# Optimization experiments

Hardware: AMD Instinct MI355X
Metric: run time of the kernel (lower is better)

The kernel has to match this reference:

```python
import jax, jax.numpy as jnp
import numpy as np

# ---- social-force / MPDM constants (param object in the original) ----
N = 4096           # number of agents (row 0 = robot)
DT = 0.4           # integration timestep [s]
PED_SPEED = 1.0    # desired pedestrian speed [m/s]
K_ATTR = 2.0       # attractive-force gain k
ALPHA = 10.0       # repulsive-force amplitude
PED_RADIUS = 0.3   # pedestrian radius [m]
PED_MASS = 60.0    # pedestrian mass [kg]
BETTA = 0.71       # repulsion range constant
A_COST = 5.0       # deviation (blame) weight a
B_COST = 2.0       # proximity-blame weight b
E_COST = 1.0       # blame length scale e
EPS = 1e-8


def calc_forces(state, goal):
    pos, vel = state[:, :2], state[:, 2:4]
    # attractive force toward goal: k * (v_desired - v_current)
    to_goal = goal - pos
    dist_g = jnp.sqrt(jnp.sum(to_goal * to_goal, axis=1, keepdims=True) + EPS)
    af = K_ATTR * (PED_SPEED * to_goal / dist_g - vel)
    # pairwise repulsive social force, [N,N,2] interaction tensor
    delta = pos[:, None, :] - pos[None, :, :]                 # [N,N,2]
    dist = jnp.sqrt(jnp.sum(delta * delta, axis=-1) + EPS)    # [N,N]
    mag = ALPHA * jnp.exp((2.0 * PED_RADIUS - dist) / BETTA)  # [N,N]
    mag = mag * (1.0 - jnp.eye(pos.shape[0], dtype=pos.dtype))  # no self-force
    rf = jnp.einsum('ij,ijc->ic', mag / dist, delta) / PED_MASS
    return rf, af


def pose_propagation(F, state):
    pos, vel = state[:, :2], state[:, 2:4]
    new_pos = pos + vel * DT + 0.5 * F * (DT * DT)
    new_vel = vel + F * DT
    spd = jnp.sqrt(jnp.sum(new_vel * new_vel, axis=1, keepdims=True) + EPS)
    new_vel = new_vel * jnp.minimum(1.0, PED_SPEED / spd)  # clamp to max speed
    return jnp.concatenate([new_pos, new_vel], axis=1)


def calc_cost_function(goal, robot_init_pose, out_state, observed_state):
    robot_pose = out_state[0, :2]
    peds = out_state[1:, :2]
    obs = observed_state[1:, :2]
    # progress of robot toward its goal
    pg = (jnp.sqrt(jnp.sum((robot_init_pose - goal[0]) ** 2) + EPS)
          - jnp.sqrt(jnp.sum((robot_pose - goal[0]) ** 2) + EPS))
    # blame: pedestrian deviation from observed trajectory
    deviation = jnp.sum(jnp.sqrt(jnp.sum((peds - obs) ** 2, axis=1) + EPS))
    # blame: robot proximity to pedestrians
    d = jnp.sqrt(jnp.sum((peds - robot_pose) ** 2, axis=1) + EPS)
    blame = jnp.sum(jnp.exp(-d / E_COST))
    return A_COST * deviation + B_COST * blame - pg


def setup_inputs() -> dict:
    key = jax.random.key(0)
    k1, k2, k3, k4 = jax.random.split(key, 4)
    pos = jax.random.normal(k1, (N, 2), dtype=jnp.float32) * 20.0
    vel = jax.random.normal(k2, (N, 2), dtype=jnp.float32)
    state = jnp.concatenate([pos, vel], axis=1)
    goal = jax.random.normal(k3, (N, 2), dtype=jnp.float32) * 20.0
    obs_pos = pos + 0.1 * jax.random.normal(k4, (N, 2), dtype=jnp.float32)
    observed_state = jnp.concatenate([obs_pos, vel], axis=1)
    return {
        'state': state,
        'cost': jnp.zeros((1,), dtype=jnp.float32),
        'stacked_trajectories_for_visualizer': state,
        'goal': goal,
        'observed_state': observed_state,
    }


def reference(state, cost, stacked_trajectories_for_visualizer, goal, observed_state):
    rf, af = calc_forces(state, goal)
    F = rf + af
    output = pose_propagation(F, state)
    temp = calc_cost_function(goal, state[0, :2], output, observed_state)
    new_cost = cost + temp
    stacked = jnp.concatenate([stacked_trajectories_for_visualizer, state], axis=0)
    return (output, new_cost, stacked)
```

## Files before the change

### kernel.cpp

```cpp
#include <hip/hip_runtime.h>

#define NPED 4096
#define SPLIT 32
#define JC (NPED / SPLIT)
#define BI 256
#define EPSF 1e-8f
#define DTF 0.4f
#define INV_MASS (1.0f/60.0f)
#define C1f (-2.0319648463225964f)
#define C0f (4.54110700268092f)
#define NLOG2E (-1.4426950408889634f)

typedef float f2 __attribute__((ext_vector_type(2)));

__device__ __forceinline__ float rsqf(float x) { return __builtin_amdgcn_rsqf(x); }
__device__ __forceinline__ float ex2(float x)  { return __builtin_amdgcn_exp2f(x); }

__global__ __launch_bounds__(BI) void forces_kernel(const float4* __restrict__ state,
                                                    const float* __restrict__ cost_in,
                                                    f2* __restrict__ part,
                                                    float* __restrict__ out) {
    __shared__ f2 spos[JC];
    const int t  = threadIdx.x;
    const int ib = blockIdx.x & 15;
    const int s  = blockIdx.x >> 4;
    if (t < JC) {
        float4 r = state[s * JC + t];
        spos[t] = (f2){r.x, r.y};
    }
    if (blockIdx.x == 0 && t == 0) out[NPED * 4] = cost_in[0];
    const int i = ib * BI + t;
    float4 mest = state[i];
    __syncthreads();
    const f2 me = {mest.x, mest.y};
    f2 acc = {0.f, 0.f};
    #pragma unroll 8
    for (int j = 0; j < JC; ++j) {
        f2 d = me - spos[j];
        float d2 = fmaf(d.x, d.x, fmaf(d.y, d.y, EPSF));
        float inv = rsqf(d2);
        float dist = d2 * inv;
        float w = ex2(fmaf(dist, C1f, C0f)) * inv;
        acc = d * w + acc;
    }
    part[s * NPED + i] = acc;
}

__device__ __forceinline__ float4 integrate_one(float4 st, float2 g,
                                                float fx, float fy) {
    fx *= INV_MASS; fy *= INV_MASS;
    float tx = g.x - st.x, ty = g.y - st.y;
    float invg = rsqf(fmaf(tx, tx, fmaf(ty, ty, EPSF)));
    float Fx = fx + 2.f * fmaf(tx, invg, -st.z);
    float Fy = fy + 2.f * fmaf(ty, invg, -st.w);
    float npx = fmaf(0.08f, Fx, fmaf(DTF, st.z, st.x));
    float npy = fmaf(0.08f, Fy, fmaf(DTF, st.w, st.y));
    float nvx = fmaf(DTF, Fx, st.z);
    float nvy = fmaf(DTF, Fy, st.w);
    float invs = rsqf(fmaf(nvx, nvx, fmaf(nvy, nvy, EPSF)));
    float sc = fminf(1.f, invs);
    return make_float4(npx, npy, nvx * sc, nvy * sc);
}

__global__ __launch_bounds__(BI) void finish_kernel(const float4* __restrict__ state,
                                                    const float2* __restrict__ goal,
                                                    const float4* __restrict__ stk,
                                                    const float* __restrict__ obs,
                                                    const f2* __restrict__ part,
                                                    float* __restrict__ out) {
    const int t  = threadIdx.x;
    const int b  = blockIdx.x;
    const int ii = b * BI + t;

    f2 f = {0.f, 0.f};
    #pragma unroll
    for (int sp = 0; sp < SPLIT; ++sp) f += part[sp * NPED + ii];
    float4 st = state[ii];
    float4 nw = integrate_one(st, goal[ii], f.x, f.y);
    ((float4*)out)[ii] = nw;

    float4 sv = stk[ii];
    float* o1 = out + (NPED * 4 + 1) + ii * 4;
    o1[0] = sv.x; o1[1] = sv.y; o1[2] = sv.z; o1[3] = sv.w;
    float* o2 = o1 + NPED * 4;
    o2[0] = st.x; o2[1] = st.y; o2[2] = st.z; o2[3] = st.w;

    __shared__ float2 rpose;
    if (t < 64) {
        f2 rf = {0.f, 0.f};
        if (t < SPLIT) rf = part[t * NPED];
        #pragma unroll
        for (int off = 16; off > 0; off >>= 1) {
            rf.x += __shfl_down(rf.x, off);
            rf.y += __shfl_down(rf.y, off);
        }
        if (t == 0) {
            float4 r0 = integrate_one(state[0], goal[0], rf.x, rf.y);
            rpose = make_float2(r0.x, r0.y);
        }
    }
    __syncthreads();
    const float rx = rpose.x, ry = rpose.y;

    float c = 0.f;
    if (ii >= 1) {
        float ox = obs[ii * 4 + 0], oy = obs[ii * 4 + 1];
        float dxo = nw.x - ox, dyo = nw.y - oy;
        float dev = sqrtf(fmaf(dxo, dxo, fmaf(dyo, dyo, EPSF)));
        float dxr = nw.x - rx, dyr = nw.y - ry;
        float d = sqrtf(fmaf(dxr, dxr, fmaf(dyr, dyr, EPSF)));
        float blame = ex2(NLOG2E * d);
        c = fmaf(5.f, dev, 2.f * blame);
    }
    #pragma unroll
    for (int off = 32; off > 0; off >>= 1) c += __shfl_down(c, off);
    __shared__ float sc4[4];
    if ((t & 63) == 0) sc4[t >> 6] = c;
    __syncthreads();
    if (t == 0) {
        float total = sc4[0] + sc4[1] + sc4[2] + sc4[3];
        if (b == 0) {
            const float* stf = (const float*)state;
            const float* gf  = (const float*)goal;
            float gx = gf[0], gy = gf[1];
            float a1x = stf[0] - gx, a1y = stf[1] - gy;
            float a2x = rx - gx,     a2y = ry - gy;
            float pg = sqrtf(fmaf(a1x, a1x, fmaf(a1y, a1y, EPSF)))
                     - sqrtf(fmaf(a2x, a2x, fmaf(a2y, a2y, EPSF)));
            total -= pg;
        }
        atomicAdd(out + NPED * 4, total);
    }
}

extern "C" void kernel_launch(void* const* d_in, const int* in_sizes, int n_in,
                              void* d_out, int out_size, void* d_ws, size_t ws_size,
                              hipStream_t stream) {
    const float4* state = (const float4*)d_in[0];
    const float*  cost  = (const float*)d_in[1];
    const float4* stk   = (const float4*)d_in[2];
    const float2* goal  = (const float2*)d_in[3];
    const float*  obs   = (const float*)d_in[4];
    float* out = (float*)d_out;
    f2* part = (f2*)d_ws;

    forces_kernel<<<dim3(16 * SPLIT), BI, 0, stream>>>(state, cost, part, out);
    finish_kernel<<<dim3(16), BI, 0, stream>>>(state, goal, stk, obs, part, out);
}
```

Before: 73.30 us.

## Split pair sum across warp lanes, fuse integration, single-block cost reduction

```diff
diff --git a/kernel.cpp b/kernel.cpp
--- a/kernel.cpp
+++ b/kernel.cpp
@@ -1,9 +1,8 @@
 #include <hip/hip_runtime.h>
 
 #define NPED 4096
-#define SPLIT 32
-#define JC (NPED / SPLIT)
 #define BI 256
+#define IPB 8
 #define EPSF 1e-8f
 #define DTF 0.4f
 #define INV_MASS (1.0f/60.0f)
@@ -15,36 +14,6 @@
 
 __device__ __forceinline__ float rsqf(float x) { return __builtin_amdgcn_rsqf(x); }
 __device__ __forceinline__ float ex2(float x)  { return __builtin_amdgcn_exp2f(x); }
-
-__global__ __launch_bounds__(BI) void forces_kernel(const float4* __restrict__ state,
-                                                    const float* __restrict__ cost_in,
-                                                    f2* __restrict__ part,
-                                                    float* __restrict__ out) {
-    __shared__ f2 spos[JC];
-    const int t  = threadIdx.x;
-    const int ib = blockIdx.x & 15;
-    const int s  = blockIdx.x >> 4;
-    if (t < JC) {
-        float4 r = state[s * JC + t];
-        spos[t] = (f2){r.x, r.y};
-    }
-    if (blockIdx.x == 0 && t == 0) out[NPED * 4] = cost_in[0];
-    const int i = ib * BI + t;
-    float4 mest = state[i];
-    __syncthreads();
-    const f2 me = {mest.x, mest.y};
-    f2 acc = {0.f, 0.f};
-    #pragma unroll 8
-    for (int j = 0; j < JC; ++j) {
-        f2 d = me - spos[j];
-        float d2 = fmaf(d.x, d.x, fmaf(d.y, d.y, EPSF));
-        float inv = rsqf(d2);
-        float dist = d2 * inv;
-        float w = ex2(fmaf(dist, C1f, C0f)) * inv;
-        acc = d * w + acc;
-    }
-    part[s * NPED + i] = acc;
-}
 
 __device__ __forceinline__ float4 integrate_one(float4 st, float2 g,
                                                 float fx, float fy) {
@@ -62,74 +31,87 @@
     return make_float4(npx, npy, nvx * sc, nvy * sc);
 }
 
-__global__ __launch_bounds__(BI) void finish_kernel(const float4* __restrict__ state,
+__global__ __launch_bounds__(BI) void forces_kernel(const float4* __restrict__ state,
                                                     const float2* __restrict__ goal,
                                                     const float4* __restrict__ stk,
-                                                    const float* __restrict__ obs,
-                                                    const f2* __restrict__ part,
                                                     float* __restrict__ out) {
-    const int t  = threadIdx.x;
-    const int b  = blockIdx.x;
-    const int ii = b * BI + t;
+    __shared__ f2 spos[NPED];
+    const int t = threadIdx.x;
+    #pragma unroll
+    for (int k = 0; k < NPED / BI; ++k) {
+        float4 r = state[k * BI + t];
+        spos[k * BI + t] = (f2){r.x, r.y};
+    }
+    const int jl = t & 31;
+    const int i  = blockIdx.x * IPB + (t >> 5);
+    float4 st = state[i];
+    __syncthreads();
 
-    f2 f = {0.f, 0.f};
+    const f2 me = {st.x, st.y};
+    f2 acc = {0.f, 0.f};
+    #pragma unroll 8
+    for (int k = 0; k < NPED / 32; ++k) {
+        f2 d = me - spos[(k << 5) + jl];
+        float d2 = fmaf(d.x, d.x, fmaf(d.y, d.y, EPSF));
+        float inv = rsqf(d2);
+        float dist = d2 * inv;
+        float w = ex2(fmaf(dist, C1f, C0f)) * inv;
+        acc = d * w + acc;
+    }
     #pragma unroll
-    for (int sp = 0; sp < SPLIT; ++sp) f += part[sp * NPED + ii];
-    float4 st = state[ii];
-    float4 nw = integrate_one(st, goal[ii], f.x, f.y);
-    ((float4*)out)[ii] = nw;
+    for (int off = 16; off > 0; off >>= 1) {
+        acc.x += __shfl_xor(acc.x, off);
+        acc.y += __shfl_xor(acc.y, off);
+    }
+    if (jl == 0) {
+        float4 nw = integrate_one(st, goal[i], acc.x, acc.y);
+        ((float4*)out)[i] = nw;
+        float4 sv = stk[i];
+        float* o1 = out + (NPED * 4 + 1) + i * 4;
+        o1[0] = sv.x; o1[1] = sv.y; o1[2] = sv.z; o1[3] = sv.w;
+        float* o2 = o1 + NPED * 4;
+        o2[0] = st.x; o2[1] = st.y; o2[2] = st.z; o2[3] = st.w;
+    }
+}
 
-    float4 sv = stk[ii];
-    float* o1 = out + (NPED * 4 + 1) + ii * 4;
-    o1[0] = sv.x; o1[1] = sv.y; o1[2] = sv.z; o1[3] = sv.w;
-    float* o2 = o1 + NPED * 4;
-    o2[0] = st.x; o2[1] = st.y; o2[2] = st.z; o2[3] = st.w;
-
-    __shared__ float2 rpose;
-    if (t < 64) {
-        f2 rf = {0.f, 0.f};
-        if (t < SPLIT) rf = part[t * NPED];
-        #pragma unroll
-        for (int off = 16; off > 0; off >>= 1) {
-            rf.x += __shfl_down(rf.x, off);
-            rf.y += __shfl_down(rf.y, off);
+__global__ __launch_bounds__(1024) void cost_kernel(const float4* __restrict__ state,
+                                                    const float2* __restrict__ goal,
+                                                    const float4* __restrict__ obs,
+                                                    const float* __restrict__ cost_in,
+                                                    float* __restrict__ out) {
+    const int t = threadIdx.x;
+    const float rx = out[0], ry = out[1];
+    float c = 0.f;
+    #pragma unroll
+    for (int k = 0; k < NPED / 1024; ++k) {
+        const int i = (k << 10) + t;
+        if (i >= 1) {
+            float4 nw = ((const float4*)out)[i];
+            float4 ob = obs[i];
+            float dxo = nw.x - ob.x, dyo = nw.y - ob.y;
+            float dev = sqrtf(fmaf(dxo, dxo, fmaf(dyo, dyo, EPSF)));
+            float dxr = nw.x - rx, dyr = nw.y - ry;
+            float d = sqrtf(fmaf(dxr, dxr, fmaf(dyr, dyr, EPSF)));
+            c = fmaf(5.f, dev, fmaf(2.f, ex2(NLOG2E * d), c));
         }
-        if (t == 0) {
-            float4 r0 = integrate_one(state[0], goal[0], rf.x, rf.y);
-            rpose = make_float2(r0.x, r0.y);
-        }
-    }
-    __syncthreads();
-    const float rx = rpose.x, ry = rpose.y;
-
-    float c = 0.f;
-    if (ii >= 1) {
-        float ox = obs[ii * 4 + 0], oy = obs[ii * 4 + 1];
-        float dxo = nw.x - ox, dyo = nw.y - oy;
-        float dev = sqrtf(fmaf(dxo, dxo, fmaf(dyo, dyo, EPSF)));
-        float dxr = nw.x - rx, dyr = nw.y - ry;
-        float d = sqrtf(fmaf(dxr, dxr, fmaf(dyr, dyr, EPSF)));
-        float blame = ex2(NLOG2E * d);
-        c = fmaf(5.f, dev, 2.f * blame);
     }
     #pragma unroll
     for (int off = 32; off > 0; off >>= 1) c += __shfl_down(c, off);
-    __shared__ float sc4[4];
-    if ((t & 63) == 0) sc4[t >> 6] = c;
+    __shared__ float wsum[16];
+    if ((t & 63) == 0) wsum[t >> 6] = c;
     __syncthreads();
     if (t == 0) {
-        float total = sc4[0] + sc4[1] + sc4[2] + sc4[3];
-        if (b == 0) {
-            const float* stf = (const float*)state;
-            const float* gf  = (const float*)goal;
-            float gx = gf[0], gy = gf[1];
-            float a1x = stf[0] - gx, a1y = stf[1] - gy;
-            float a2x = rx - gx,     a2y = ry - gy;
-            float pg = sqrtf(fmaf(a1x, a1x, fmaf(a1y, a1y, EPSF)))
-                     - sqrtf(fmaf(a2x, a2x, fmaf(a2y, a2y, EPSF)));
-            total -= pg;
-        }
-        atomicAdd(out + NPED * 4, total);
+        float tot = 0.f;
+        #pragma unroll
+        for (int w = 0; w < 16; ++w) tot += wsum[w];
+        const float* stf = (const float*)state;
+        const float* gf  = (const float*)goal;
+        float gx = gf[0], gy = gf[1];
+        float a1x = stf[0] - gx, a1y = stf[1] - gy;
+        float a2x = rx - gx,     a2y = ry - gy;
+        float pg = sqrtf(fmaf(a1x, a1x, fmaf(a1y, a1y, EPSF)))
+                 - sqrtf(fmaf(a2x, a2x, fmaf(a2y, a2y, EPSF)));
+        out[NPED * 4] = cost_in[0] + tot - pg;
     }
 }
 
@@ -140,10 +122,9 @@
     const float*  cost  = (const float*)d_in[1];
     const float4* stk   = (const float4*)d_in[2];
     const float2* goal  = (const float2*)d_in[3];
-    const float*  obs   = (const float*)d_in[4];
+    const float4* obs   = (const float4*)d_in[4];
     float* out = (float*)d_out;
-    f2* part = (f2*)d_ws;
 
-    forces_kernel<<<dim3(16 * SPLIT), BI, 0, stream>>>(state, cost, part, out);
-    finish_kernel<<<dim3(16), BI, 0, stream>>>(state, goal, stk, obs, part, out);
+    forces_kernel<<<dim3(NPED / IPB), BI, 0, stream>>>(state, goal, stk, out);
+    cost_kernel<<<dim3(1), 1024, 0, stream>>>(state, goal, obs, cost, out);
 }
```

Result: no change. 74.39 us (+1.5%).
